# Kernel optimization log

Hardware: AMD Instinct MI355X
Metric: run time of the kernel (lower is better)

## Reference

```python
import jax, jax.numpy as jnp
import numpy as np

N, T = 20000, 8
E = 320000
HID, HEADS = 128, 2
HPC = HID // HEADS  # hid channels per head (concat=True)
NEG_SLOPE = 0.2  # PyG GATv2Conv default


def setup_inputs() -> dict:
    key = jax.random.key(0)
    ks = jax.random.split(key, 16)
    s = 0.1
    return {
        "x": jax.random.normal(ks[0], (N, T), dtype=jnp.float32),
        "edge_index": jax.random.randint(ks[1], (2, E), 0, N, dtype=jnp.int64),
        "edge_weight": jax.random.uniform(ks[2], (E,), dtype=jnp.float32),
        # GATv2Conv params (in_channels=1 -> heads*hpc)
        "W_l": jax.random.normal(ks[3], (1, HID), dtype=jnp.float32) * s,
        "b_l": jnp.zeros((HID,), jnp.float32),
        "W_r": jax.random.normal(ks[4], (1, HID), dtype=jnp.float32) * s,
        "b_r": jnp.zeros((HID,), jnp.float32),
        "att": jax.random.normal(ks[5], (HEADS, HPC), dtype=jnp.float32) * s,
        "conv_bias": jnp.zeros((HID,), jnp.float32),
        # GRU-style gate params
        "W1": jax.random.normal(ks[6], (2 * HID, 2 * HID), dtype=jnp.float32) * s,
        "b1": jnp.zeros((2 * HID,), jnp.float32),
        "W2": jax.random.normal(ks[7], (2 * HID, HID), dtype=jnp.float32) * s,
        "b2": jnp.zeros((HID,), jnp.float32),
    }


def _gatv2(xt, src, dst, n, W_l, b_l, W_r, b_r, att, conv_bias):
    H, C = att.shape
    xl = (xt @ W_l + b_l).reshape(n, H, C)  # source transform
    xr = (xt @ W_r + b_r).reshape(n, H, C)  # target transform
    g = jax.nn.leaky_relu(xl[src] + xr[dst], NEG_SLOPE)  # [E', H, C]
    e = jnp.einsum('ehc,hc->eh', g, att)  # attention logits
    # softmax over incoming edges of each destination node
    emax = jax.ops.segment_max(e, dst, num_segments=n)
    ex = jnp.exp(e - emax[dst])
    denom = jax.ops.segment_sum(ex, dst, num_segments=n)
    alpha = ex / (denom[dst] + 1e-16)  # [E', H]
    msg = alpha[:, :, None] * xl[src]
    out = jax.ops.segment_sum(msg, dst, num_segments=n)  # [N, H, C]
    return out.reshape(n, H * C) + conv_bias


def reference(x, edge_index, edge_weight, W_l, b_l, W_r, b_r, att, conv_bias, W1, b1, W2, b2):
    n = x.shape[0]
    # GATv2Conv default add_self_loops=True
    loops = jnp.arange(n, dtype=edge_index.dtype)
    src = jnp.concatenate([edge_index[0], loops])
    dst = jnp.concatenate([edge_index[1], loops])

    def step(h, xt_col):
        xt = xt_col[:, None]  # [N, 1]
        f = jax.nn.sigmoid(_gatv2(xt, src, dst, n, W_l, b_l, W_r, b_r, att, conv_bias))
        ru = jax.nn.sigmoid(jnp.concatenate([f, h], axis=1) @ W1 + b1)
        r, u = jnp.split(ru, 2, axis=1)
        c = jnp.tanh(jnp.concatenate([f, r * h], axis=1) @ W2 + b2)
        h_new = u * h + (1.0 - u) * c
        return h_new, None

    h0 = jnp.zeros((n, HID), dtype=x.dtype)
    h, _ = jax.lax.scan(jax.checkpoint(step), h0, x.T)  # scan over time
    return h
```

## Files before the change

### kernel.cpp

```cpp
#include <hip/hip_runtime.h>
#include <hip/hip_bf16.h>

#define N_NODES 20000
#define T_STEPS 8
#define E_EDGES 320000
#define HID 128
#define BN 80

typedef short short8 __attribute__((ext_vector_type(8)));
typedef float f32x4 __attribute__((ext_vector_type(4)));

__device__ __attribute__((aligned(16))) float g_xT[T_STEPS * N_NODES];
__device__ __attribute__((aligned(16))) float g_ndf[T_STEPS * N_NODES * 4];
__device__ __attribute__((aligned(16))) int   g_cnt[N_NODES];
__device__ __attribute__((aligned(16))) int   g_rowptr[N_NODES + 1];
__device__ __attribute__((aligned(16))) int   g_cursor[N_NODES];
__device__ __attribute__((aligned(16))) int   g_sorted[E_EDGES];
__device__ __attribute__((aligned(16))) short g_w1hi[65536];
__device__ __attribute__((aligned(16))) short g_w1lo[65536];
__device__ __attribute__((aligned(16))) short g_w2hi[32768];
__device__ __attribute__((aligned(16))) short g_w2lo[32768];
__device__ float g_lin[6];
__device__ int   g_flag;

__device__ __forceinline__ float fsig(float z) {
    return 1.0f / (1.0f + __expf(-z));
}
__device__ __forceinline__ unsigned short f2bf(float f) {
    unsigned u = __builtin_bit_cast(unsigned, f);
    unsigned r = (u + 0x7FFFu + ((u >> 16) & 1u)) >> 16;
    return (unsigned short)r;
}
__device__ __forceinline__ float bf2f(unsigned short s) {
    return __builtin_bit_cast(float, ((unsigned)s) << 16);
}

__global__ __launch_bounds__(256) void init_kernel(
    const float* __restrict__ x, const unsigned int* __restrict__ ei32)
{
    const int i = blockIdx.x * 256 + threadIdx.x;
    if (i < T_STEPS * N_NODES) {
        const int n = i >> 3, t = i & 7;
        g_xT[t * N_NODES + n] = x[i];
    }
    if (i < N_NODES) g_cnt[i] = 0;
    if (i == 0) {
        int all_zero = 1;
        for (int k = 0; k < 64; ++k)
            if (ei32[2 * k + 1] != 0u) { all_zero = 0; break; }
        g_flag = all_zero;
    }
}

__device__ __forceinline__ void load_edge(const void* ei, int e, int& src, int& dst) {
    if (g_flag) {
        const long long* p = (const long long*)ei;
        src = (int)p[e]; dst = (int)p[E_EDGES + e];
    } else {
        const int* p = (const int*)ei;
        src = p[e]; dst = p[E_EDGES + e];
    }
}

__global__ __launch_bounds__(256) void hist_kernel(const void* __restrict__ ei) {
    const int e = blockIdx.x * 256 + threadIdx.x;
    if (e >= E_EDGES) return;
    int src, dst; load_edge(ei, e, src, dst);
    atomicAdd(&g_cnt[dst], 1);
}

__global__ __launch_bounds__(1024) void scan_kernel() {
    __shared__ int part[1024];
    const int tid  = threadIdx.x;
    const int base = tid * 20;
    int local[20];
    int s = 0;
    #pragma unroll
    for (int i = 0; i < 20; ++i) {
        const int n = base + i;
        const int c = (n < N_NODES) ? g_cnt[n] : 0;
        local[i] = s; s += c;
    }
    part[tid] = s;
    __syncthreads();
    for (int off = 1; off < 1024; off <<= 1) {
        const int v = (tid >= off) ? part[tid - off] : 0;
        __syncthreads();
        part[tid] += v;
        __syncthreads();
    }
    const int pre = (tid == 0) ? 0 : part[tid - 1];
    #pragma unroll
    for (int i = 0; i < 20; ++i) {
        const int n = base + i;
        if (n < N_NODES) {
            const int v = pre + local[i];
            g_rowptr[n] = v;
            g_cursor[n] = v;
        }
    }
    if (tid == 1023) g_rowptr[N_NODES] = part[1023];
}

__global__ __launch_bounds__(256) void scatter_kernel(const void* __restrict__ ei) {
    const int e = blockIdx.x * 256 + threadIdx.x;
    if (e >= E_EDGES) return;
    int src, dst; load_edge(ei, e, src, dst);
    const int pos = atomicAdd(&g_cursor[dst], 1);
    g_sorted[pos] = src;
}

__global__ __launch_bounds__(256) void prep_kernel(
    const float* __restrict__ W1, const float* __restrict__ W2,
    const float* __restrict__ W_l, const float* __restrict__ b_l,
    const float* __restrict__ W_r, const float* __restrict__ b_r,
    const float* __restrict__ att)
{
    int i = blockIdx.x * 256 + threadIdx.x;
    if (i < 65536) {
        int k = i >> 8, n = i & 255;
        float w = W1[i];
        int kb = k >> 5, kq = (k >> 3) & 3, r = k & 7;
        int idx = ((kb * 256 + n) * 4 + kq) * 8 + r;
        unsigned short hi = f2bf(w);
        g_w1hi[idx] = (short)hi;
        g_w1lo[idx] = (short)f2bf(w - bf2f(hi));
    } else {
        int j = i - 65536;
        int k = j >> 7, n = j & 127;
        float w = W2[j];
        int kb = k >> 5, kq = (k >> 3) & 3, r = k & 7;
        int idx = ((kb * 128 + n) * 4 + kq) * 8 + r;
        unsigned short hi = f2bf(w);
        g_w2hi[idx] = (short)hi;
        g_w2lo[idx] = (short)f2bf(w - bf2f(hi));
    }
    if (blockIdx.x == 0 && threadIdx.x < 2) {
        const int hh = threadIdx.x;
        float P = 0.f, Q = 0.f, R = 0.f;
        for (int k = 0; k < 64; ++k) {
            const int c = hh * 64 + k;
            const float a = att[c];
            P = fmaf(a, W_l[c], P);
            Q = fmaf(a, W_r[c], Q);
            R = fmaf(a, b_l[c] + b_r[c], R);
        }
        g_lin[hh * 3 + 0] = P;
        g_lin[hh * 3 + 1] = Q;
        g_lin[hh * 3 + 2] = R;
    }
}

__global__ __launch_bounds__(256) void edge_all_kernel(
    const float* __restrict__ W_l, const float* __restrict__ b_l,
    const float* __restrict__ W_r, const float* __restrict__ b_r,
    const float* __restrict__ att)
{
    __shared__ float4 ch4[128];
    const int tid = threadIdx.x;
    if (tid < 128)
        ch4[tid] = make_float4(W_l[tid], W_r[tid], b_l[tid] + b_r[tid], att[tid]);
    __syncthreads();

    const int n    = blockIdx.x * 128 + (tid >> 1);
    const int head = tid & 1;
    const int t    = blockIdx.y;
    if (n >= N_NODES) return;

    const float* xrow = &g_xT[t * N_NODES];
    const float xd = xrow[n];
    const float P = g_lin[head * 3 + 0];
    const float Q = g_lin[head * 3 + 1];
    const float R = g_lin[head * 3 + 2];
    const float4* chh = &ch4[head * 64];

    const int base = g_rowptr[n];
    const int deg  = g_rowptr[n + 1] - base;
    const int tot  = deg + 1;

    float den = 0.f, num = 0.f;
    for (int cs = 0; cs < tot; cs += 8) {
        int m = tot - cs; if (m > 8) m = 8;
        float xs[8];
        #pragma unroll
        for (int e = 0; e < 8; ++e) {
            xs[e] = 0.f;
            if (e < m) {
                const int idx = cs + e;
                xs[e] = (idx == 0) ? xd : xrow[g_sorted[base + idx - 1]];
            }
        }
        float ea[8];
        #pragma unroll
        for (int e = 0; e < 8; ++e) ea[e] = 0.f;
        #pragma unroll 4
        for (int c = 0; c < 64; ++c) {
            const float4 f = chh[c];
            const float dpart = fmaf(xd, f.y, f.z);
            #pragma unroll
            for (int e = 0; e < 8; ++e) {
                const float a = fmaf(xs[e], f.x, dpart);
                ea[e] = fmaf(fabsf(a), f.w, ea[e]);
            }
        }
        #pragma unroll
        for (int e = 0; e < 8; ++e) {
            if (e < m) {
                const float ee = fmaf(0.6f, fmaf(xs[e], P, fmaf(xd, Q, R)), 0.4f * ea[e]);
                const float ex = __expf(ee);
                den += ex;
                num = fmaf(ex, xs[e], num);
            }
        }
    }
    g_ndf[((size_t)t * N_NODES + n) * 4 + head]     = den;
    g_ndf[((size_t)t * N_NODES + n) * 4 + 2 + head] = num;
}

__global__ __launch_bounds__(512) void gru_all_kernel(
    const float* __restrict__ W_l, const float* __restrict__ b_l,
    const float* __restrict__ conv_bias,
    const float* __restrict__ b1, const float* __restrict__ b2,
    float* __restrict__ hout)
{
    __shared__ short featA[BN * 256];
    __shared__ float hbuf[BN * HID];
    __shared__ float swl[128], sbl[128], scb[128], sb1a[128], sb1b[128], sb2[128];

    const int t   = threadIdx.x;
    const int n0g = blockIdx.x * BN;

    if (t < 128) {
        swl[t] = W_l[t]; sbl[t] = b_l[t]; scb[t] = conv_bias[t];
        sb1a[t] = b1[t]; sb1b[t] = b1[128 + t]; sb2[t] = b2[t];
    }
    for (int i = t; i < BN * HID; i += 512) hbuf[i] = 0.f;
    for (int i = t; i < BN * 16; i += 512) {
        const int node = i >> 4;
        const int g    = 16 + (i & 15);
        const int gsw  = g ^ (node & 7);
        *(short8*)&featA[node * 256 + gsw * 8] = (short8)0;
    }

    const int wid = t >> 6;
    const int l   = t & 63;
    const int lr  = l & 15;
    const int lk  = l >> 4;
    const int ec  = wid * 16 + lr;

    f32x4 uh[5], us[5];

    for (int step = 0; step < T_STEPS; ++step) {
        for (int G = t; G < BN * 16; G += 512) {
            const int node = G >> 4;
            const int g    = G & 15;
            const int head = g >> 3;
            const size_t bi = ((size_t)step * N_NODES + n0g + node) * 4;
            const float den = g_ndf[bi + head];
            const float num = g_ndf[bi + 2 + head];
            const float inv = 1.0f / (den + 1e-16f);
            short8 v;
            #pragma unroll
            for (int r = 0; r < 8; ++r) {
                const int c = g * 8 + r;
                const float z = (num * swl[c] + den * sbl[c]) * inv + scb[c];
                v[r] = (short)f2bf(fsig(z));
            }
            const int gsw = g ^ (node & 7);
            *(short8*)&featA[node * 256 + gsw * 8] = v;
        }
        __syncthreads();

        f32x4 acc[5][2];
        {
            const float ba = sb1a[ec], bb = sb1b[ec];
            #pragma unroll
            for (int mf = 0; mf < 5; ++mf) {
                acc[mf][0] = (f32x4){ba, ba, ba, ba};
                acc[mf][1] = (f32x4){bb, bb, bb, bb};
            }
        }
        #pragma unroll
        for (int kb = 0; kb < 8; ++kb) {
            short8 ah[5];
            #pragma unroll
            for (int mf = 0; mf < 5; ++mf) {
                const int row = mf * 16 + lr;
                const int g   = (kb * 4 + lk) ^ (row & 7);
                ah[mf] = *(short8*)&featA[row * 256 + g * 8];
            }
            const int bidx0 = ((kb * 256 + ec) * 4 + lk) * 8;
            const int bidx1 = ((kb * 256 + 128 + ec) * 4 + lk) * 8;
            const short8 bh0 = *(const short8*)&g_w1hi[bidx0];
            const short8 bl0 = *(const short8*)&g_w1lo[bidx0];
            const short8 bh1 = *(const short8*)&g_w1hi[bidx1];
            const short8 bl1 = *(const short8*)&g_w1lo[bidx1];
            #pragma unroll
            for (int mf = 0; mf < 5; ++mf) {
                acc[mf][0] = __builtin_amdgcn_mfma_f32_16x16x32_bf16(ah[mf], bh0, acc[mf][0], 0, 0, 0);
                acc[mf][0] = __builtin_amdgcn_mfma_f32_16x16x32_bf16(ah[mf], bl0, acc[mf][0], 0, 0, 0);
                acc[mf][1] = __builtin_amdgcn_mfma_f32_16x16x32_bf16(ah[mf], bh1, acc[mf][1], 0, 0, 0);
                acc[mf][1] = __builtin_amdgcn_mfma_f32_16x16x32_bf16(ah[mf], bl1, acc[mf][1], 0, 0, 0);
            }
        }
        __syncthreads();

        #pragma unroll
        for (int mf = 0; mf < 5; ++mf) {
            #pragma unroll
            for (int j = 0; j < 4; ++j) {
                const int row = mf * 16 + lk * 4 + j;
                const float r = fsig(acc[mf][0][j]);
                const float u = fsig(acc[mf][1][j]);
                const float h32 = hbuf[row * HID + ec];
                uh[mf][j] = u * h32;
                us[mf][j] = u;
                const int colk = 128 + ec;
                const int g = (colk >> 3) ^ (row & 7);
                featA[row * 256 + g * 8 + (colk & 7)] = (short)f2bf(r * h32);
            }
        }
        __syncthreads();

        f32x4 acc2[5];
        {
            const float bb = sb2[ec];
            #pragma unroll
            for (int mf = 0; mf < 5; ++mf)
                acc2[mf] = (f32x4){bb, bb, bb, bb};
        }
        #pragma unroll
        for (int kb = 0; kb < 8; ++kb) {
            short8 ah[5];
            #pragma unroll
            for (int mf = 0; mf < 5; ++mf) {
                const int row = mf * 16 + lr;
                const int g   = (kb * 4 + lk) ^ (row & 7);
                ah[mf] = *(short8*)&featA[row * 256 + g * 8];
            }
            const int bidx = ((kb * 128 + ec) * 4 + lk) * 8;
            const short8 bh = *(const short8*)&g_w2hi[bidx];
            const short8 bl = *(const short8*)&g_w2lo[bidx];
            #pragma unroll
            for (int mf = 0; mf < 5; ++mf) {
                acc2[mf] = __builtin_amdgcn_mfma_f32_16x16x32_bf16(ah[mf], bh, acc2[mf], 0, 0, 0);
                acc2[mf] = __builtin_amdgcn_mfma_f32_16x16x32_bf16(ah[mf], bl, acc2[mf], 0, 0, 0);
            }
        }
        __syncthreads();

        #pragma unroll
        for (int mf = 0; mf < 5; ++mf) {
            #pragma unroll
            for (int j = 0; j < 4; ++j) {
                const int row = mf * 16 + lk * 4 + j;
                const float c  = tanhf(acc2[mf][j]);
                const float hn = uh[mf][j] + c - us[mf][j] * c;
                if (step < T_STEPS - 1) {
                    hbuf[row * HID + ec] = hn;
                    const int colk = 128 + ec;
                    const int g = (colk >> 3) ^ (row & 7);
                    featA[row * 256 + g * 8 + (colk & 7)] = (short)f2bf(hn);
                } else {
                    hout[(size_t)(n0g + row) * HID + ec] = hn;
                }
            }
        }
    }
}

extern "C" void kernel_launch(void* const* d_in, const int* in_sizes, int n_in,
                              void* d_out, int out_size, void* d_ws, size_t ws_size,
                              hipStream_t stream) {
    const float* x   = (const float*)d_in[0];
    const void*  ei  = d_in[1];
    const float* W_l = (const float*)d_in[3];
    const float* b_l = (const float*)d_in[4];
    const float* W_r = (const float*)d_in[5];
    const float* b_r = (const float*)d_in[6];
    const float* att = (const float*)d_in[7];
    const float* cb  = (const float*)d_in[8];
    const float* W1  = (const float*)d_in[9];
    const float* b1  = (const float*)d_in[10];
    const float* W2  = (const float*)d_in[11];
    const float* b2  = (const float*)d_in[12];

    float* h = (float*)d_out;
    (void)d_ws; (void)ws_size;

    init_kernel<<<(T_STEPS * N_NODES + 255) / 256, 256, 0, stream>>>(
        x, (const unsigned int*)ei);
    hist_kernel<<<(E_EDGES + 255) / 256, 256, 0, stream>>>(ei);
    scan_kernel<<<1, 1024, 0, stream>>>();
    scatter_kernel<<<(E_EDGES + 255) / 256, 256, 0, stream>>>(ei);
    prep_kernel<<<384, 256, 0, stream>>>(W1, W2, W_l, b_l, W_r, b_r, att);
    edge_all_kernel<<<dim3(157, T_STEPS), 256, 0, stream>>>(W_l, b_l, W_r, b_r, att);
    gru_all_kernel<<<N_NODES / BN, 512, 0, stream>>>(W_l, b_l, cb, b1, b2, h);
}
```

Baseline: 327.1 us.

## Shrink GRU node tile, keep hidden state in registers, double-buffer feature LDS

The GRU kernel now processes 32 nodes per block instead of 80 and asks for four blocks per CU through launch bounds. The hidden state stays in registers rather than an LDS buffer. Feature columns are double-buffered by step parity so two barriers per step can be dropped, and bf16 writes are packed in pairs with a lane shuffle. Separately, edge-dtype detection moves into its own single-thread kernel. The aim is more blocks in flight, less LDS traffic and fewer syncs, at the cost of one extra kernel launch and less reuse of the W1/W2 weight loads per block.

```diff
diff --git a/kernel.cpp b/kernel.cpp
--- a/kernel.cpp
+++ b/kernel.cpp
@@ -5,7 +5,7 @@
 #define T_STEPS 8
 #define E_EDGES 320000
 #define HID 128
-#define BN 80
+#define BN 32
 
 typedef short short8 __attribute__((ext_vector_type(8)));
 typedef float f32x4 __attribute__((ext_vector_type(4)));
@@ -35,21 +35,11 @@
     return __builtin_bit_cast(float, ((unsigned)s) << 16);
 }
 
-__global__ __launch_bounds__(256) void init_kernel(
-    const float* __restrict__ x, const unsigned int* __restrict__ ei32)
-{
-    const int i = blockIdx.x * 256 + threadIdx.x;
-    if (i < T_STEPS * N_NODES) {
-        const int n = i >> 3, t = i & 7;
-        g_xT[t * N_NODES + n] = x[i];
-    }
-    if (i < N_NODES) g_cnt[i] = 0;
-    if (i == 0) {
-        int all_zero = 1;
-        for (int k = 0; k < 64; ++k)
-            if (ei32[2 * k + 1] != 0u) { all_zero = 0; break; }
-        g_flag = all_zero;
-    }
+__global__ void detect_kernel(const unsigned int* __restrict__ ei32) {
+    int all_zero = 1;
+    for (int k = 0; k < 64; ++k)
+        if (ei32[2 * k + 1] != 0u) { all_zero = 0; break; }
+    g_flag = all_zero;
 }
 
 __device__ __forceinline__ void load_edge(const void* ei, int e, int& src, int& dst) {
@@ -60,6 +50,18 @@
         const int* p = (const int*)ei;
         src = p[e]; dst = p[E_EDGES + e];
     }
+}
+
+__global__ __launch_bounds__(256) void init_kernel(
+    const float* __restrict__ x, const void* __restrict__ ei)
+{
+    const int i = blockIdx.x * 256 + threadIdx.x;
+    if (i < T_STEPS * N_NODES) {
+        const int n = i >> 3, t = i & 7;
+        g_xT[t * N_NODES + n] = x[i];
+    }
+    if (i < N_NODES) g_cnt[i] = 0;
+    __threadfence();
 }
 
 __global__ __launch_bounds__(256) void hist_kernel(const void* __restrict__ ei) {
@@ -217,14 +219,13 @@
     g_ndf[((size_t)t * N_NODES + n) * 4 + 2 + head] = num;
 }
 
-__global__ __launch_bounds__(512) void gru_all_kernel(
+__global__ __launch_bounds__(512, 4) void gru_all_kernel(
     const float* __restrict__ W_l, const float* __restrict__ b_l,
     const float* __restrict__ conv_bias,
     const float* __restrict__ b1, const float* __restrict__ b2,
     float* __restrict__ hout)
 {
-    __shared__ short featA[BN * 256];
-    __shared__ float hbuf[BN * HID];
+    __shared__ short featA[BN * 512];
     __shared__ float swl[128], sbl[128], scb[128], sb1a[128], sb1b[128], sb2[128];
 
     const int t   = threadIdx.x;
@@ -234,133 +235,142 @@
         swl[t] = W_l[t]; sbl[t] = b_l[t]; scb[t] = conv_bias[t];
         sb1a[t] = b1[t]; sb1b[t] = b1[128 + t]; sb2[t] = b2[t];
     }
-    for (int i = t; i < BN * HID; i += 512) hbuf[i] = 0.f;
-    for (int i = t; i < BN * 16; i += 512) {
-        const int node = i >> 4;
-        const int g    = 16 + (i & 15);
+    {
+        const int node = t >> 4;
+        const int g    = 16 + (t & 15);
         const int gsw  = g ^ (node & 7);
-        *(short8*)&featA[node * 256 + gsw * 8] = (short8)0;
-    }
+        *(short8*)&featA[node * 512 + gsw * 8] = (short8)0;
+    }
+    __syncthreads();
 
     const int wid = t >> 6;
     const int l   = t & 63;
     const int lr  = l & 15;
     const int lk  = l >> 4;
     const int ec  = wid * 16 + lr;
-
-    f32x4 uh[5], us[5];
+    const int pnode = t >> 4;
+    const int pg    = t & 15;
+
+    const float ba1 = sb1a[ec], bb1 = sb1b[ec], bb2 = sb2[ec];
+
+    f32x4 hreg[2], ureg[2];
+    hreg[0] = (f32x4){0.f, 0.f, 0.f, 0.f};
+    hreg[1] = (f32x4){0.f, 0.f, 0.f, 0.f};
 
     for (int step = 0; step < T_STEPS; ++step) {
-        for (int G = t; G < BN * 16; G += 512) {
-            const int node = G >> 4;
-            const int g    = G & 15;
-            const int head = g >> 3;
-            const size_t bi = ((size_t)step * N_NODES + n0g + node) * 4;
+        const int fbase = (step & 1) ? 48 : 0;
+
+        {
+            const int head = pg >> 3;
+            const size_t bi = ((size_t)step * N_NODES + n0g + pnode) * 4;
             const float den = g_ndf[bi + head];
             const float num = g_ndf[bi + 2 + head];
             const float inv = 1.0f / (den + 1e-16f);
             short8 v;
             #pragma unroll
             for (int r = 0; r < 8; ++r) {
-                const int c = g * 8 + r;
+                const int c = pg * 8 + r;
                 const float z = (num * swl[c] + den * sbl[c]) * inv + scb[c];
                 v[r] = (short)f2bf(fsig(z));
             }
-            const int gsw = g ^ (node & 7);
-            *(short8*)&featA[node * 256 + gsw * 8] = v;
+            const int gsw = (fbase + pg) ^ (pnode & 7);
+            *(short8*)&featA[pnode * 512 + gsw * 8] = v;
         }
         __syncthreads();
 
-        f32x4 acc[5][2];
-        {
-            const float ba = sb1a[ec], bb = sb1b[ec];
-            #pragma unroll
-            for (int mf = 0; mf < 5; ++mf) {
-                acc[mf][0] = (f32x4){ba, ba, ba, ba};
-                acc[mf][1] = (f32x4){bb, bb, bb, bb};
-            }
+        f32x4 acc0[2], acc1[2];
+        #pragma unroll
+        for (int mf = 0; mf < 2; ++mf) {
+            acc0[mf] = (f32x4){ba1, ba1, ba1, ba1};
+            acc1[mf] = (f32x4){bb1, bb1, bb1, bb1};
         }
         #pragma unroll
         for (int kb = 0; kb < 8; ++kb) {
-            short8 ah[5];
-            #pragma unroll
-            for (int mf = 0; mf < 5; ++mf) {
+            const int glin = kb * 4 + lk;
+            const int gra  = (glin < 16) ? fbase + glin : glin;
+            short8 ah[2];
+            #pragma unroll
+            for (int mf = 0; mf < 2; ++mf) {
                 const int row = mf * 16 + lr;
-                const int g   = (kb * 4 + lk) ^ (row & 7);
-                ah[mf] = *(short8*)&featA[row * 256 + g * 8];
+                const int g   = gra ^ (row & 7);
+                ah[mf] = *(short8*)&featA[row * 512 + g * 8];
             }
             const int bidx0 = ((kb * 256 + ec) * 4 + lk) * 8;
-            const int bidx1 = ((kb * 256 + 128 + ec) * 4 + lk) * 8;
+            const int bidx1 = bidx0 + 4096;
             const short8 bh0 = *(const short8*)&g_w1hi[bidx0];
             const short8 bl0 = *(const short8*)&g_w1lo[bidx0];
             const short8 bh1 = *(const short8*)&g_w1hi[bidx1];
             const short8 bl1 = *(const short8*)&g_w1lo[bidx1];
             #pragma unroll
-            for (int mf = 0; mf < 5; ++mf) {
-                acc[mf][0] = __builtin_amdgcn_mfma_f32_16x16x32_bf16(ah[mf], bh0, acc[mf][0], 0, 0, 0);
-                acc[mf][0] = __builtin_amdgcn_mfma_f32_16x16x32_bf16(ah[mf], bl0, acc[mf][0], 0, 0, 0);
-                acc[mf][1] = __builtin_amdgcn_mfma_f32_16x16x32_bf16(ah[mf], bh1, acc[mf][1], 0, 0, 0);
-                acc[mf][1] = __builtin_amdgcn_mfma_f32_16x16x32_bf16(ah[mf], bl1, acc[mf][1], 0, 0, 0);
-            }
-        }
-        __syncthreads();
-
-        #pragma unroll
-        for (int mf = 0; mf < 5; ++mf) {
+            for (int mf = 0; mf < 2; ++mf) {
+                acc0[mf] = __builtin_amdgcn_mfma_f32_16x16x32_bf16(ah[mf], bh0, acc0[mf], 0, 0, 0);
+                acc0[mf] = __builtin_amdgcn_mfma_f32_16x16x32_bf16(ah[mf], bl0, acc0[mf], 0, 0, 0);
+                acc1[mf] = __builtin_amdgcn_mfma_f32_16x16x32_bf16(ah[mf], bh1, acc1[mf], 0, 0, 0);
+                acc1[mf] = __builtin_amdgcn_mfma_f32_16x16x32_bf16(ah[mf], bl1, acc1[mf], 0, 0, 0);
+            }
+        }
+
+        #pragma unroll
+        for (int mf = 0; mf < 2; ++mf) {
             #pragma unroll
             for (int j = 0; j < 4; ++j) {
                 const int row = mf * 16 + lk * 4 + j;
-                const float r = fsig(acc[mf][0][j]);
-                const float u = fsig(acc[mf][1][j]);
-                const float h32 = hbuf[row * HID + ec];
-                uh[mf][j] = u * h32;
-                us[mf][j] = u;
-                const int colk = 128 + ec;
-                const int g = (colk >> 3) ^ (row & 7);
-                featA[row * 256 + g * 8 + (colk & 7)] = (short)f2bf(r * h32);
+                const float r = fsig(acc0[mf][j]);
+                const float u = fsig(acc1[mf][j]);
+                ureg[mf][j] = u;
+                const float rh = r * hreg[mf][j];
+                const float ot = __shfl_xor(rh, 1);
+                if ((lr & 1) == 0) {
+                    const unsigned pk = (unsigned)f2bf(rh) | ((unsigned)f2bf(ot) << 16);
+                    const int g  = (32 + (ec >> 3)) ^ (row & 7);
+                    const int ad = row * 512 + g * 8 + (ec & 7);
+                    *(unsigned*)&featA[ad] = pk;
+                }
             }
         }
         __syncthreads();
 
-        f32x4 acc2[5];
-        {
-            const float bb = sb2[ec];
-            #pragma unroll
-            for (int mf = 0; mf < 5; ++mf)
-                acc2[mf] = (f32x4){bb, bb, bb, bb};
-        }
+        f32x4 acc2[2];
+        #pragma unroll
+        for (int mf = 0; mf < 2; ++mf)
+            acc2[mf] = (f32x4){bb2, bb2, bb2, bb2};
         #pragma unroll
         for (int kb = 0; kb < 8; ++kb) {
-            short8 ah[5];
-            #pragma unroll
-            for (int mf = 0; mf < 5; ++mf) {
+            const int glin = kb * 4 + lk;
+            const int gra  = (glin < 16) ? fbase + glin : glin + 16;
+            short8 ah[2];
+            #pragma unroll
+            for (int mf = 0; mf < 2; ++mf) {
                 const int row = mf * 16 + lr;
-                const int g   = (kb * 4 + lk) ^ (row & 7);
-                ah[mf] = *(short8*)&featA[row * 256 + g * 8];
+                const int g   = gra ^ (row & 7);
+                ah[mf] = *(short8*)&featA[row * 512 + g * 8];
             }
             const int bidx = ((kb * 128 + ec) * 4 + lk) * 8;
             const short8 bh = *(const short8*)&g_w2hi[bidx];
             const short8 bl = *(const short8*)&g_w2lo[bidx];
             #pragma unroll
-            for (int mf = 0; mf < 5; ++mf) {
+            for (int mf = 0; mf < 2; ++mf) {
                 acc2[mf] = __builtin_amdgcn_mfma_f32_16x16x32_bf16(ah[mf], bh, acc2[mf], 0, 0, 0);
                 acc2[mf] = __builtin_amdgcn_mfma_f32_16x16x32_bf16(ah[mf], bl, acc2[mf], 0, 0, 0);
             }
         }
-        __syncthreads();
-
-        #pragma unroll
-        for (int mf = 0; mf < 5; ++mf) {
+
+        #pragma unroll
+        for (int mf = 0; mf < 2; ++mf) {
             #pragma unroll
             for (int j = 0; j < 4; ++j) {
                 const int row = mf * 16 + lk * 4 + j;
                 const float c  = tanhf(acc2[mf][j]);
-                const float hn = uh[mf][j] + c - us[mf][j] * c;
+                const float hn = fmaf(ureg[mf][j], hreg[mf][j] - c, c);
+                hreg[mf][j] = hn;
                 if (step < T_STEPS - 1) {
-                    hbuf[row * HID + ec] = hn;
-                    const int colk = 128 + ec;
-                    const int g = (colk >> 3) ^ (row & 7);
-                    featA[row * 256 + g * 8 + (colk & 7)] = (short)f2bf(hn);
+                    const float ot = __shfl_xor(hn, 1);
+                    if ((lr & 1) == 0) {
+                        const unsigned pk = (unsigned)f2bf(hn) | ((unsigned)f2bf(ot) << 16);
+                        const int g  = (16 + (ec >> 3)) ^ (row & 7);
+                        const int ad = row * 512 + g * 8 + (ec & 7);
+                        *(unsigned*)&featA[ad] = pk;
+                    }
                 } else {
                     hout[(size_t)(n0g + row) * HID + ec] = hn;
                 }
@@ -388,8 +398,8 @@
     float* h = (float*)d_out;
     (void)d_ws; (void)ws_size;
 
-    init_kernel<<<(T_STEPS * N_NODES + 255) / 256, 256, 0, stream>>>(
-        x, (const unsigned int*)ei);
+    detect_kernel<<<1, 1, 0, stream>>>((const unsigned int*)ei);
+    init_kernel<<<(T_STEPS * N_NODES + 255) / 256, 256, 0, stream>>>(x, ei);
     hist_kernel<<<(E_EDGES + 255) / 256, 256, 0, stream>>>(ei);
     scan_kernel<<<1, 1024, 0, stream>>>();
     scatter_kernel<<<(E_EDGES + 255) / 256, 256, 0, stream>>>(ei);
```

Measured after the change: 580.2 us. 77.4% more time.

## Split GRU gates across 16 waves with K-split second GEMM and register-held state

Applied to the files above, without the earlier changes.

The GRU kernel goes from 512 to 1024 threads. Each wave now computes either the r or the u half of the first GEMM, and the second GEMM is split over K, with partial sums combined through a shared-memory buffer. Hidden state now lives in registers instead of a shared float buffer, u is stored as bf16 in shared memory, and LDS writes are packed in pairs via lane shuffles. This aims to double per-block parallelism and cut per-wave MFMA chains, at the cost of more shared memory, an extra partial-sum exchange and possible occupancy loss. The edge-format detection is also moved into its own single-thread kernel, which adds a launch.

```diff
diff --git a/kernel.cpp b/kernel.cpp
--- a/kernel.cpp
+++ b/kernel.cpp
@@ -35,21 +35,11 @@
     return __builtin_bit_cast(float, ((unsigned)s) << 16);
 }
 
-__global__ __launch_bounds__(256) void init_kernel(
-    const float* __restrict__ x, const unsigned int* __restrict__ ei32)
-{
-    const int i = blockIdx.x * 256 + threadIdx.x;
-    if (i < T_STEPS * N_NODES) {
-        const int n = i >> 3, t = i & 7;
-        g_xT[t * N_NODES + n] = x[i];
-    }
-    if (i < N_NODES) g_cnt[i] = 0;
-    if (i == 0) {
-        int all_zero = 1;
-        for (int k = 0; k < 64; ++k)
-            if (ei32[2 * k + 1] != 0u) { all_zero = 0; break; }
-        g_flag = all_zero;
-    }
+__global__ void detect_kernel(const unsigned int* __restrict__ ei32) {
+    int all_zero = 1;
+    for (int k = 0; k < 64; ++k)
+        if (ei32[2 * k + 1] != 0u) { all_zero = 0; break; }
+    g_flag = all_zero;
 }
 
 __device__ __forceinline__ void load_edge(const void* ei, int e, int& src, int& dst) {
@@ -60,6 +50,17 @@
         const int* p = (const int*)ei;
         src = p[e]; dst = p[E_EDGES + e];
     }
+}
+
+__global__ __launch_bounds__(256) void init_kernel(
+    const float* __restrict__ x, const void* __restrict__ ei)
+{
+    const int i = blockIdx.x * 256 + threadIdx.x;
+    if (i < T_STEPS * N_NODES) {
+        const int n = i >> 3, t = i & 7;
+        g_xT[t * N_NODES + n] = x[i];
+    }
+    if (i < N_NODES) g_cnt[i] = 0;
 }
 
 __global__ __launch_bounds__(256) void hist_kernel(const void* __restrict__ ei) {
@@ -217,14 +218,15 @@
     g_ndf[((size_t)t * N_NODES + n) * 4 + 2 + head] = num;
 }
 
-__global__ __launch_bounds__(512) void gru_all_kernel(
+__global__ __launch_bounds__(1024) void gru_all_kernel(
     const float* __restrict__ W_l, const float* __restrict__ b_l,
     const float* __restrict__ conv_bias,
     const float* __restrict__ b1, const float* __restrict__ b2,
     float* __restrict__ hout)
 {
-    __shared__ short featA[BN * 256];
-    __shared__ float hbuf[BN * HID];
+    __shared__ short featA[BN * 384];
+    __shared__ short ubuf[BN * 136];
+    __shared__ float pbuf[BN * 132];
     __shared__ float swl[128], sbl[128], scb[128], sb1a[128], sb1b[128], sb2[128];
 
     const int t   = threadIdx.x;
@@ -234,27 +236,35 @@
         swl[t] = W_l[t]; sbl[t] = b_l[t]; scb[t] = conv_bias[t];
         sb1a[t] = b1[t]; sb1b[t] = b1[128 + t]; sb2[t] = b2[t];
     }
-    for (int i = t; i < BN * HID; i += 512) hbuf[i] = 0.f;
-    for (int i = t; i < BN * 16; i += 512) {
+    for (int i = t; i < BN * 16; i += 1024) {
         const int node = i >> 4;
         const int g    = 16 + (i & 15);
         const int gsw  = g ^ (node & 7);
-        *(short8*)&featA[node * 256 + gsw * 8] = (short8)0;
-    }
+        *(short8*)&featA[node * 384 + gsw * 8] = (short8)0;
+    }
+    __syncthreads();
 
     const int wid = t >> 6;
     const int l   = t & 63;
     const int lr  = l & 15;
     const int lk  = l >> 4;
-    const int ec  = wid * 16 + lr;
-
-    f32x4 uh[5], us[5];
+    const bool rw = (wid < 8);
+    const int ec  = (wid & 7) * 16 + lr;
+    const int c1  = ((wid >> 3) << 7) + ec;
+    const int kb0 = (wid >> 3) * 4;
+
+    const float bias1 = rw ? sb1a[ec] : sb1b[ec];
+    const float bias2 = rw ? sb2[ec] : 0.f;
+
+    f32x4 hreg[5];
+    #pragma unroll
+    for (int mf = 0; mf < 5; ++mf) hreg[mf] = (f32x4){0.f, 0.f, 0.f, 0.f};
 
     for (int step = 0; step < T_STEPS; ++step) {
-        for (int G = t; G < BN * 16; G += 512) {
+        for (int G = t; G < BN * 16; G += 1024) {
             const int node = G >> 4;
-            const int g    = G & 15;
-            const int head = g >> 3;
+            const int pg   = G & 15;
+            const int head = pg >> 3;
             const size_t bi = ((size_t)step * N_NODES + n0g + node) * 4;
             const float den = g_ndf[bi + head];
             const float num = g_ndf[bi + 2 + head];
@@ -262,107 +272,133 @@
             short8 v;
             #pragma unroll
             for (int r = 0; r < 8; ++r) {
-                const int c = g * 8 + r;
+                const int c = pg * 8 + r;
                 const float z = (num * swl[c] + den * sbl[c]) * inv + scb[c];
                 v[r] = (short)f2bf(fsig(z));
             }
-            const int gsw = g ^ (node & 7);
-            *(short8*)&featA[node * 256 + gsw * 8] = v;
+            const int gsw = pg ^ (node & 7);
+            *(short8*)&featA[node * 384 + gsw * 8] = v;
         }
         __syncthreads();
 
-        f32x4 acc[5][2];
+        f32x4 acc[5];
+        #pragma unroll
+        for (int mf = 0; mf < 5; ++mf)
+            acc[mf] = (f32x4){bias1, bias1, bias1, bias1};
+        #pragma unroll
+        for (int half = 0; half < 2; ++half) {
+            short8 wB[8];
+            #pragma unroll
+            for (int i = 0; i < 4; ++i) {
+                const int kb = half * 4 + i;
+                const int bidx = ((kb * 256 + c1) * 4 + lk) * 8;
+                wB[2 * i]     = *(const short8*)&g_w1hi[bidx];
+                wB[2 * i + 1] = *(const short8*)&g_w1lo[bidx];
+            }
+            #pragma unroll
+            for (int i = 0; i < 4; ++i) {
+                const int glin = (half * 4 + i) * 4 + lk;
+                #pragma unroll
+                for (int mf = 0; mf < 5; ++mf) {
+                    const int row = mf * 16 + lr;
+                    const short8 ah = *(short8*)&featA[row * 384 + (glin ^ (row & 7)) * 8];
+                    acc[mf] = __builtin_amdgcn_mfma_f32_16x16x32_bf16(ah, wB[2 * i], acc[mf], 0, 0, 0);
+                    acc[mf] = __builtin_amdgcn_mfma_f32_16x16x32_bf16(ah, wB[2 * i + 1], acc[mf], 0, 0, 0);
+                }
+            }
+        }
+
+        if (rw) {
+            #pragma unroll
+            for (int mf = 0; mf < 5; ++mf) {
+                #pragma unroll
+                for (int j = 0; j < 4; ++j) {
+                    const int row = mf * 16 + lk * 4 + j;
+                    const float r  = fsig(acc[mf][j]);
+                    const float rh = r * hreg[mf][j];
+                    const float ot = __shfl_xor(rh, 1);
+                    if ((lr & 1) == 0) {
+                        const unsigned pk = (unsigned)f2bf(rh) | ((unsigned)f2bf(ot) << 16);
+                        const int g  = (32 + (ec >> 3)) ^ (row & 7);
+                        *(unsigned*)&featA[row * 384 + g * 8 + (ec & 7)] = pk;
+                    }
+                }
+            }
+        } else {
+            #pragma unroll
+            for (int mf = 0; mf < 5; ++mf) {
+                #pragma unroll
+                for (int j = 0; j < 4; ++j) {
+                    const int row = mf * 16 + lk * 4 + j;
+                    const float u  = fsig(acc[mf][j]);
+                    const float ot = __shfl_xor(u, 1);
+                    if ((lr & 1) == 0) {
+                        const unsigned pk = (unsigned)f2bf(u) | ((unsigned)f2bf(ot) << 16);
+                        *(unsigned*)&ubuf[row * 136 + ec] = pk;
+                    }
+                }
+            }
+        }
+        __syncthreads();
+
+        f32x4 acc2[5];
+        #pragma unroll
+        for (int mf = 0; mf < 5; ++mf)
+            acc2[mf] = (f32x4){bias2, bias2, bias2, bias2};
         {
-            const float ba = sb1a[ec], bb = sb1b[ec];
+            short8 vB[8];
+            #pragma unroll
+            for (int i = 0; i < 4; ++i) {
+                const int bidx = (((kb0 + i) * 128 + ec) * 4 + lk) * 8;
+                vB[2 * i]     = *(const short8*)&g_w2hi[bidx];
+                vB[2 * i + 1] = *(const short8*)&g_w2lo[bidx];
+            }
+            #pragma unroll
+            for (int i = 0; i < 4; ++i) {
+                const int glin = (kb0 + i) * 4 + lk;
+                const int gra  = (glin < 16) ? glin : glin + 16;
+                #pragma unroll
+                for (int mf = 0; mf < 5; ++mf) {
+                    const int row = mf * 16 + lr;
+                    const short8 ah = *(short8*)&featA[row * 384 + (gra ^ (row & 7)) * 8];
+                    acc2[mf] = __builtin_amdgcn_mfma_f32_16x16x32_bf16(ah, vB[2 * i], acc2[mf], 0, 0, 0);
+                    acc2[mf] = __builtin_amdgcn_mfma_f32_16x16x32_bf16(ah, vB[2 * i + 1], acc2[mf], 0, 0, 0);
+                }
+            }
+        }
+        if (!rw) {
             #pragma unroll
             for (int mf = 0; mf < 5; ++mf) {
-                acc[mf][0] = (f32x4){ba, ba, ba, ba};
-                acc[mf][1] = (f32x4){bb, bb, bb, bb};
-            }
-        }
-        #pragma unroll
-        for (int kb = 0; kb < 8; ++kb) {
-            short8 ah[5];
+                #pragma unroll
+                for (int j = 0; j < 4; ++j) {
+                    const int row = mf * 16 + lk * 4 + j;
+                    pbuf[row * 132 + ec] = acc2[mf][j];
+                }
+            }
+        }
+        __syncthreads();
+
+        if (rw) {
             #pragma unroll
             for (int mf = 0; mf < 5; ++mf) {
-                const int row = mf * 16 + lr;
-                const int g   = (kb * 4 + lk) ^ (row & 7);
-                ah[mf] = *(short8*)&featA[row * 256 + g * 8];
-            }
-            const int bidx0 = ((kb * 256 + ec) * 4 + lk) * 8;
-            const int bidx1 = ((kb * 256 + 128 + ec) * 4 + lk) * 8;
-            const short8 bh0 = *(const short8*)&g_w1hi[bidx0];
-            const short8 bl0 = *(const short8*)&g_w1lo[bidx0];
-            const short8 bh1 = *(const short8*)&g_w1hi[bidx1];
-            const short8 bl1 = *(const short8*)&g_w1lo[bidx1];
-            #pragma unroll
-            for (int mf = 0; mf < 5; ++mf) {
-                acc[mf][0] = __builtin_amdgcn_mfma_f32_16x16x32_bf16(ah[mf], bh0, acc[mf][0], 0, 0, 0);
-                acc[mf][0] = __builtin_amdgcn_mfma_f32_16x16x32_bf16(ah[mf], bl0, acc[mf][0], 0, 0, 0);
-                acc[mf][1] = __builtin_amdgcn_mfma_f32_16x16x32_bf16(ah[mf], bh1, acc[mf][1], 0, 0, 0);
-                acc[mf][1] = __builtin_amdgcn_mfma_f32_16x16x32_bf16(ah[mf], bl1, acc[mf][1], 0, 0, 0);
-            }
-        }
-        __syncthreads();
-
-        #pragma unroll
-        for (int mf = 0; mf < 5; ++mf) {
-            #pragma unroll
-            for (int j = 0; j < 4; ++j) {
-                const int row = mf * 16 + lk * 4 + j;
-                const float r = fsig(acc[mf][0][j]);
-                const float u = fsig(acc[mf][1][j]);
-                const float h32 = hbuf[row * HID + ec];
-                uh[mf][j] = u * h32;
-                us[mf][j] = u;
-                const int colk = 128 + ec;
-                const int g = (colk >> 3) ^ (row & 7);
-                featA[row * 256 + g * 8 + (colk & 7)] = (short)f2bf(r * h32);
-            }
-        }
-        __syncthreads();
-
-        f32x4 acc2[5];
-        {
-            const float bb = sb2[ec];
-            #pragma unroll
-            for (int mf = 0; mf < 5; ++mf)
-                acc2[mf] = (f32x4){bb, bb, bb, bb};
-        }
-        #pragma unroll
-        for (int kb = 0; kb < 8; ++kb) {
-            short8 ah[5];
-            #pragma unroll
-            for (int mf = 0; mf < 5; ++mf) {
-                const int row = mf * 16 + lr;
-                const int g   = (kb * 4 + lk) ^ (row & 7);
-                ah[mf] = *(short8*)&featA[row * 256 + g * 8];
-            }
-            const int bidx = ((kb * 128 + ec) * 4 + lk) * 8;
-            const short8 bh = *(const short8*)&g_w2hi[bidx];
-            const short8 bl = *(const short8*)&g_w2lo[bidx];
-            #pragma unroll
-            for (int mf = 0; mf < 5; ++mf) {
-                acc2[mf] = __builtin_amdgcn_mfma_f32_16x16x32_bf16(ah[mf], bh, acc2[mf], 0, 0, 0);
-                acc2[mf] = __builtin_amdgcn_mfma_f32_16x16x32_bf16(ah[mf], bl, acc2[mf], 0, 0, 0);
-            }
-        }
-        __syncthreads();
-
-        #pragma unroll
-        for (int mf = 0; mf < 5; ++mf) {
-            #pragma unroll
-            for (int j = 0; j < 4; ++j) {
-                const int row = mf * 16 + lk * 4 + j;
-                const float c  = tanhf(acc2[mf][j]);
-                const float hn = uh[mf][j] + c - us[mf][j] * c;
-                if (step < T_STEPS - 1) {
-                    hbuf[row * HID + ec] = hn;
-                    const int colk = 128 + ec;
-                    const int g = (colk >> 3) ^ (row & 7);
-                    featA[row * 256 + g * 8 + (colk & 7)] = (short)f2bf(hn);
-                } else {
-                    hout[(size_t)(n0g + row) * HID + ec] = hn;
+                #pragma unroll
+                for (int j = 0; j < 4; ++j) {
+                    const int row = mf * 16 + lk * 4 + j;
+                    const float zc = acc2[mf][j] + pbuf[row * 132 + ec];
+                    const float c  = tanhf(zc);
+                    const float u  = bf2f((unsigned short)ubuf[row * 136 + ec]);
+                    const float hn = fmaf(u, hreg[mf][j] - c, c);
+                    hreg[mf][j] = hn;
+                    if (step < T_STEPS - 1) {
+                        const float ot = __shfl_xor(hn, 1);
+                        if ((lr & 1) == 0) {
+                            const unsigned pk = (unsigned)f2bf(hn) | ((unsigned)f2bf(ot) << 16);
+                            const int g  = (16 + (ec >> 3)) ^ (row & 7);
+                            *(unsigned*)&featA[row * 384 + g * 8 + (ec & 7)] = pk;
+                        }
+                    } else {
+                        hout[(size_t)(n0g + row) * HID + ec] = hn;
+                    }
                 }
             }
         }
@@ -388,12 +424,12 @@
     float* h = (float*)d_out;
     (void)d_ws; (void)ws_size;
 
-    init_kernel<<<(T_STEPS * N_NODES + 255) / 256, 256, 0, stream>>>(
-        x, (const unsigned int*)ei);
+    detect_kernel<<<1, 1, 0, stream>>>((const unsigned int*)ei);
+    init_kernel<<<(T_STEPS * N_NODES + 255) / 256, 256, 0, stream>>>(x, ei);
     hist_kernel<<<(E_EDGES + 255) / 256, 256, 0, stream>>>(ei);
     scan_kernel<<<1, 1024, 0, stream>>>();
     scatter_kernel<<<(E_EDGES + 255) / 256, 256, 0, stream>>>(ei);
     prep_kernel<<<384, 256, 0, stream>>>(W1, W2, W_l, b_l, W_r, b_r, att);
     edge_all_kernel<<<dim3(157, T_STEPS), 256, 0, stream>>>(W_l, b_l, W_r, b_r, att);
-    gru_all_kernel<<<N_NODES / BN, 512, 0, stream>>>(W_l, b_l, cb, b1, b2, h);
-}
+    gru_all_kernel<<<N_NODES / BN, 1024, 0, stream>>>(W_l, b_l, cb, b1, b2, h);
+}
```

Result: slower. 435.5 us (+33.1%).
